# Kernel tuning notes

Hardware: AMD Instinct MI355X
Metric: run time of the kernel (lower is better)

Reference implementation:

```python
import jax, jax.numpy as jnp
import numpy as np

TOP_K = 2

def _expert(x, w1, w2, w3):
    return (jax.nn.silu(x @ w1.T) * (x @ w3.T)) @ w2.T

def setup_inputs() -> dict:
    key = jax.random.key(0)
    ks = jax.random.split(key, 8)
    B, L, D, F, E, S = 4, 2048, 1024, 512, 16, 1
    p = lambda k, shape: (jax.random.normal(k, shape, jnp.float32) * 0.02)
    return {
        "x": jax.random.normal(ks[0], (B, L, D), jnp.float32),
        "gate_w": p(ks[1], (E, D)),
        "expert_bias": jnp.zeros((E,), jnp.float32),
        "sw1": p(ks[2], (S, F, D)),
        "sw2": p(ks[3], (S, D, F)),
        "sw3": p(ks[4], (S, F, D)),
        "ew1": p(ks[5], (E, F, D)),
        "ew2": p(ks[6], (E, D, F)),
        "ew3": p(ks[7], (E, F, D)),
    }

def reference(x, gate_w, expert_bias, sw1, sw2, sw3, ew1, ew2, ew3):
    B, L, D = x.shape
    E = gate_w.shape[0]
    flat_x = x.reshape(-1, D)  # [T, D], T = B*L

    # Shared experts (always-on)
    shared = sum(_expert(flat_x, sw1[i], sw2[i], sw3[i]) for i in range(sw1.shape[0]))

    # Router (eval mode: no jitter noise, no bias update; expert_bias buffer added)
    logits = flat_x @ gate_w.T + expert_bias          # [T, E]
    probs = jax.nn.softmax(logits, axis=-1)
    topw, topi = jax.lax.top_k(probs, TOP_K)          # [T, k]
    topw = topw / jnp.sum(topw, axis=-1, keepdims=True)

    # Routed experts: combine weight per (token, expert); zero weight => zero contribution,
    # identical math to the masked gather/scatter in the original.
    out = jnp.zeros_like(flat_x)
    for e in range(E):  # fixed small structural loop over experts
        cw = jnp.sum(jnp.where(topi == e, topw, 0.0), axis=-1)  # [T]
        out = out + cw[:, None] * _expert(flat_x, ew1[e], ew2[e], ew3[e])

    y = (shared + out).reshape(B, L, D)
    return y, probs
```

## Files before the change

### kernel.cpp

```cpp
#include <hip/hip_runtime.h>

typedef unsigned short u16;
typedef __bf16 bf16_t;
typedef bf16_t bf16x8 __attribute__((ext_vector_type(8)));
typedef float f32x4 __attribute__((ext_vector_type(4)));

#define T_TOK 8192
#define DIM   1024
#define FF    512
#define NE    16
#define RBASE_SHARED (2 * T_TOK)
#define NROWS (RBASE_SHARED + T_TOK)
#define MAXTILES 256
#define NSEG 512

__device__ __forceinline__ u16 f2bf(float f) {
  union { float f; unsigned u; } v; v.f = f;
  unsigned r = v.u + 0x7FFFu + ((v.u >> 16) & 1u);
  return (u16)(r >> 16);
}
__device__ __forceinline__ float bf2f(u16 h) {
  union { unsigned u; float f; } v; v.u = ((unsigned)h) << 16; return v.f;
}
__device__ __forceinline__ int clampi(int v, int lo, int hi) {
  return v < lo ? lo : (v > hi ? hi : v);
}

#define GLL16(g, l) __builtin_amdgcn_global_load_lds( \
    (const __attribute__((address_space(1))) void*)(g), \
    (__attribute__((address_space(3))) void*)(l), 16, 0, 0)

#define X4   2097152
#define SW4  131072
#define EW4  2097152
#define TOT4 (X4 + 3 * SW4 + 3 * EW4)

__global__ __launch_bounds__(256) void cvt_all_kernel(
    const float* __restrict__ x, const float* __restrict__ sw1,
    const float* __restrict__ sw2, const float* __restrict__ sw3,
    const float* __restrict__ ew1, const float* __restrict__ ew2,
    const float* __restrict__ ew3,
    u16* __restrict__ xb, u16* __restrict__ sw1b, u16* __restrict__ sw2b,
    u16* __restrict__ sw3b, u16* __restrict__ ew1b, u16* __restrict__ ew2b,
    u16* __restrict__ ew3b) {
  int i = blockIdx.x * 256 + threadIdx.x;
  const float* s; u16* dst; int j;
  if (i < X4)                       { s = x;   dst = xb;   j = i; }
  else if (i < X4 + SW4)            { s = sw1; dst = sw1b; j = i - X4; }
  else if (i < X4 + 2 * SW4)        { s = sw2; dst = sw2b; j = i - (X4 + SW4); }
  else if (i < X4 + 3 * SW4)        { s = sw3; dst = sw3b; j = i - (X4 + 2 * SW4); }
  else if (i < X4 + 3 * SW4 + EW4)      { s = ew1; dst = ew1b; j = i - (X4 + 3 * SW4); }
  else if (i < X4 + 3 * SW4 + 2 * EW4)  { s = ew2; dst = ew2b; j = i - (X4 + 3 * SW4 + EW4); }
  else if (i < TOT4)                    { s = ew3; dst = ew3b; j = i - (X4 + 3 * SW4 + 2 * EW4); }
  else return;
  float4 v = reinterpret_cast<const float4*>(s)[j];
  ushort4 o;
  o.x = f2bf(v.x); o.y = f2bf(v.y); o.z = f2bf(v.z); o.w = f2bf(v.w);
  reinterpret_cast<ushort4*>(dst)[j] = o;
}

__global__ __launch_bounds__(256) void router_kernel(
    const float* __restrict__ x, const float* __restrict__ gw,
    const float* __restrict__ ebias, float* __restrict__ probs,
    int* __restrict__ topi, float* __restrict__ topw, int* __restrict__ cnt_seg) {
  __shared__ int hist[16];
  int tid = threadIdx.x;
  int lane = tid & 63, w = tid >> 6;
  if (tid < 16) hist[tid] = 0;
  __syncthreads();
  const float4* gv = reinterpret_cast<const float4*>(gw);
  for (int it = 0; it < 2; ++it) {
    int t0 = blockIdx.x * 16 + (w + 4 * it) * 2;
    const float4* x0 = reinterpret_cast<const float4*>(x + (size_t)t0 * DIM);
    const float4* x1 = reinterpret_cast<const float4*>(x + (size_t)(t0 + 1) * DIM);
    float4 xa[4], xc[4];
#pragma unroll
    for (int j = 0; j < 4; ++j) { xa[j] = x0[j * 64 + lane]; xc[j] = x1[j * 64 + lane]; }
    float p0[16], p1[16];
#pragma unroll
    for (int e = 0; e < NE; ++e) {
      float s0 = 0.f, s1 = 0.f;
#pragma unroll
      for (int j = 0; j < 4; ++j) {
        float4 g = gv[e * 256 + j * 64 + lane];
        s0 += xa[j].x * g.x + xa[j].y * g.y + xa[j].z * g.z + xa[j].w * g.w;
        s1 += xc[j].x * g.x + xc[j].y * g.y + xc[j].z * g.z + xc[j].w * g.w;
      }
#pragma unroll
      for (int d = 1; d < 64; d <<= 1) { s0 += __shfl_xor(s0, d); s1 += __shfl_xor(s1, d); }
      float b = ebias[e];
      p0[e] = s0 + b; p1[e] = s1 + b;
    }
    float m0 = p0[0], m1 = p1[0];
#pragma unroll
    for (int e = 1; e < NE; ++e) { m0 = fmaxf(m0, p0[e]); m1 = fmaxf(m1, p1[e]); }
    float sum0 = 0.f, sum1 = 0.f;
#pragma unroll
    for (int e = 0; e < NE; ++e) {
      p0[e] = __expf(p0[e] - m0); sum0 += p0[e];
      p1[e] = __expf(p1[e] - m1); sum1 += p1[e];
    }
    float inv0 = 1.f / sum0, inv1 = 1.f / sum1;
#pragma unroll
    for (int e = 0; e < NE; ++e) { p0[e] *= inv0; p1[e] *= inv1; }
    if (lane == 0) {
#pragma unroll
      for (int j = 0; j < 4; ++j)
        reinterpret_cast<float4*>(probs + (size_t)t0 * NE)[j] =
            make_float4(p0[4 * j], p0[4 * j + 1], p0[4 * j + 2], p0[4 * j + 3]);
      float b1 = -1.f, b2 = -1.f; int i1 = 0, i2 = 0;
#pragma unroll
      for (int e = 0; e < NE; ++e) {
        float pe = p0[e];
        if (pe > b1) { b2 = b1; i2 = i1; b1 = pe; i1 = e; }
        else if (pe > b2) { b2 = pe; i2 = e; }
      }
      float ws = b1 + b2;
      reinterpret_cast<int2*>(topi)[t0] = make_int2(i1, i2);
      reinterpret_cast<float2*>(topw)[t0] = make_float2(b1 / ws, b2 / ws);
      atomicAdd(&hist[i1], 1); atomicAdd(&hist[i2], 1);
    }
    if (lane == 1) {
      int t1 = t0 + 1;
#pragma unroll
      for (int j = 0; j < 4; ++j)
        reinterpret_cast<float4*>(probs + (size_t)t1 * NE)[j] =
            make_float4(p1[4 * j], p1[4 * j + 1], p1[4 * j + 2], p1[4 * j + 3]);
      float b1 = -1.f, b2 = -1.f; int i1 = 0, i2 = 0;
#pragma unroll
      for (int e = 0; e < NE; ++e) {
        float pe = p1[e];
        if (pe > b1) { b2 = b1; i2 = i1; b1 = pe; i1 = e; }
        else if (pe > b2) { b2 = pe; i2 = e; }
      }
      float ws = b1 + b2;
      reinterpret_cast<int2*>(topi)[t1] = make_int2(i1, i2);
      reinterpret_cast<float2*>(topw)[t1] = make_float2(b1 / ws, b2 / ws);
      atomicAdd(&hist[i1], 1); atomicAdd(&hist[i2], 1);
    }
  }
  __syncthreads();
  if (tid < 16) cnt_seg[blockIdx.x * 16 + tid] = hist[tid];
}

__global__ __launch_bounds__(256) void scan_kernel(
    const int* __restrict__ cnt_seg, int* __restrict__ cnt, int* __restrict__ offs,
    int* __restrict__ seg_base, int2* __restrict__ tab) {
  __shared__ int chunk_sum[16][16];
  __shared__ int chunk_base[16][16];
  __shared__ int tot[16], off_s[17];
  int tid = threadIdx.x;
  int e = tid & 15, c = tid >> 4;
  int s0 = 0;
  for (int s = 0; s < 32; ++s) s0 += cnt_seg[(c * 32 + s) * 16 + e];
  chunk_sum[c][e] = s0;
  __syncthreads();
  if (tid < 16) {
    int r = 0;
    for (int c2 = 0; c2 < 16; ++c2) { chunk_base[c2][tid] = r; r += chunk_sum[c2][tid]; }
    tot[tid] = r;
  }
  __syncthreads();
  if (tid == 0) {
    int a = 0;
    for (int i = 0; i < 16; ++i) { off_s[i] = a; offs[i] = a; cnt[i] = tot[i]; a += tot[i]; }
    off_s[16] = RBASE_SHARED; offs[16] = RBASE_SHARED;
    int n = 0;
    for (int g = 0; g <= 16 && n < MAXTILES; ++g) {
      int M = (g == 16) ? T_TOK : tot[g];
      for (int m0 = 0; m0 < M && n < MAXTILES; m0 += 128) { tab[n] = make_int2(g, m0); ++n; }
    }
    for (; n < MAXTILES; ++n) tab[n] = make_int2(-1, 0);
  }
  __syncthreads();
  int r = off_s[e] + chunk_base[c][e];
  for (int s = 0; s < 32; ++s) {
    int seg = c * 32 + s;
    seg_base[seg * 16 + e] = r;
    r += cnt_seg[seg * 16 + e];
  }
}

__global__ __launch_bounds__(64) void scatter_kernel(
    const int* __restrict__ topi, const float* __restrict__ topw,
    const int* __restrict__ seg_base,
    int* __restrict__ idx, float* __restrict__ cwl, int* __restrict__ slotmap) {
  __shared__ int ti[16][2]; __shared__ float tw[16][2]; __shared__ int base[16];
  int b = blockIdx.x;
  int tid = threadIdx.x;
  if (tid < 16) {
    int t = b * 16 + tid;
    int2 pp = reinterpret_cast<const int2*>(topi)[t];
    ti[tid][0] = clampi(pp.x, 0, 15); ti[tid][1] = clampi(pp.y, 0, 15);
    float2 ww = reinterpret_cast<const float2*>(topw)[t];
    tw[tid][0] = ww.x; tw[tid][1] = ww.y;
    base[tid] = seg_base[b * 16 + tid];
  }
  __syncthreads();
  if (tid < 32) {
    int l = tid >> 1, s = tid & 1;
    int t = b * 16 + l;
    int e = ti[l][s];
    int rank = 0;
    for (int t2 = 0; t2 < 16; ++t2) {
      if (ti[t2][0] == e && (t2 < l || (t2 == l && 0 < s))) ++rank;
      if (ti[t2][1] == e && (t2 < l)) ++rank;
    }
    int slot = clampi(base[e] + rank, 0, NROWS - 1);
    idx[slot] = t; cwl[slot] = tw[l][s]; slotmap[t * 3 + s] = slot;
  } else if (tid < 48) {
    int l = tid - 32;
    int t = b * 16 + l;
    int sh = RBASE_SHARED + t;
    idx[sh] = t; cwl[sh] = 1.0f; slotmap[t * 3 + 2] = sh;
  }
}

__global__ __launch_bounds__(256) void gemm_silu_kernel(
    const u16* __restrict__ A, const u16* __restrict__ sw1b, const u16* __restrict__ sw3b,
    const u16* __restrict__ ew1b, const u16* __restrict__ ew3b, u16* __restrict__ G,
    const int2* __restrict__ tab, const int* __restrict__ offs,
    const int* __restrict__ cnt, const int* __restrict__ gidx) {
  const int K = DIM;
  int nwg = gridDim.x * gridDim.y;
  int orig = blockIdx.x + gridDim.x * blockIdx.y;
  int per = nwg >> 3;
  int wg = (orig & 7) * per + (orig >> 3);
  int tileid = wg & (MAXTILES - 1);
  int ny = wg >> 8;
  int2 te = tab[tileid];
  int e = te.x;
  if (e < 0) return;
  e = clampi(e, 0, NE);
  int m0 = te.y;
  int M = (e == NE) ? T_TOK : cnt[e];
  M = clampi(M, 1, T_TOK);
  int rowbase = clampi(offs[e], 0, NROWS - 1);
  const u16* B1 = (e == NE) ? sw1b : ew1b + (size_t)e * FF * K;
  const u16* B3 = (e == NE) ? sw3b : ew3b + (size_t)e * FF * K;
  int n0 = ny * 128;

  __shared__ u16 As[2 * 4096], B1s[2 * 4096], B3s[2 * 4096];

  int tid = threadIdx.x;
  int lane = tid & 63, wv = tid >> 6;
  int srow = tid >> 2, sg = tid & 3;
  int sk0 = (sg ^ ((srow >> 1) & 3)) * 8;
  int sk1 = (sg ^ (((srow + 64) >> 1) & 3)) * 8;
  int r0 = min(m0 + srow, M - 1);
  int r1 = min(m0 + srow + 64, M - 1);
  int ga0 = clampi(gidx[clampi(rowbase + r0, 0, NROWS - 1)], 0, T_TOK - 1);
  int ga1 = clampi(gidx[clampi(rowbase + r1, 0, NROWS - 1)], 0, T_TOK - 1);
  const u16* Ap0 = A + (size_t)ga0 * K + sk0;
  const u16* Ap1 = A + (size_t)ga1 * K + sk1;
  const u16* B1p0 = B1 + (size_t)(n0 + srow) * K + sk0;
  const u16* B1p1 = B1 + (size_t)(n0 + srow + 64) * K + sk1;
  const u16* B3p0 = B3 + (size_t)(n0 + srow) * K + sk0;
  const u16* B3p1 = B3 + (size_t)(n0 + srow + 64) * K + sk1;
  int st0 = wv * 512, st1 = 2048 + wv * 512;

  int ln15 = lane & 15, qd = lane >> 4;
  int qsw = (qd ^ ((ln15 >> 1) & 3)) * 8;
  int wm = (wv >> 1) * 64, wn = (wv & 1) * 64;
  int aoff = (wm + ln15) * 32 + qsw;
  int boff = (wn + ln15) * 32 + qsw;

  f32x4 acc1[4][4] = {};
  f32x4 acc3[4][4] = {};

  const int nk = K / 32;
  GLL16(Ap0, As + st0);        GLL16(Ap1, As + st1);
  GLL16(B1p0, B1s + st0);      GLL16(B1p1, B1s + st1);
  GLL16(B3p0, B3s + st0);      GLL16(B3p1, B3s + st1);
  __syncthreads();
#pragma unroll 2
  for (int t = 0; t < nk; ++t) {
    int cur = (t & 1) * 4096;
    if (t + 1 < nk) {
      int nxt = ((t + 1) & 1) * 4096;
      int kt = (t + 1) * 32;
      GLL16(Ap0 + kt, As + nxt + st0);     GLL16(Ap1 + kt, As + nxt + st1);
      GLL16(B1p0 + kt, B1s + nxt + st0);   GLL16(B1p1 + kt, B1s + nxt + st1);
      GLL16(B3p0 + kt, B3s + nxt + st0);   GLL16(B3p1 + kt, B3s + nxt + st1);
    }
    bf16x8 af[4], b1f[4], b3f[4];
#pragma unroll
    for (int i = 0; i < 4; ++i) {
      af[i]  = *reinterpret_cast<const bf16x8*>(&As[cur + aoff + i * 512]);
      b1f[i] = *reinterpret_cast<const bf16x8*>(&B1s[cur + boff + i * 512]);
      b3f[i] = *reinterpret_cast<const bf16x8*>(&B3s[cur + boff + i * 512]);
    }
#pragma unroll
    for (int i = 0; i < 4; ++i)
#pragma unroll
      for (int j = 0; j < 4; ++j) {
        acc1[i][j] = __builtin_amdgcn_mfma_f32_16x16x32_bf16(af[i], b1f[j], acc1[i][j], 0, 0, 0);
        acc3[i][j] = __builtin_amdgcn_mfma_f32_16x16x32_bf16(af[i], b3f[j], acc3[i][j], 0, 0, 0);
      }
    __syncthreads();
  }

  int mrem = M - m0;
#pragma unroll
  for (int i = 0; i < 4; ++i)
#pragma unroll
    for (int r = 0; r < 4; ++r) {
      int ml = wm + i * 16 + qd * 4 + r;
      if (ml < mrem) {
        size_t orow = (size_t)clampi(rowbase + m0 + ml, 0, NROWS - 1);
#pragma unroll
        for (int j = 0; j < 4; ++j) {
          float z1 = acc1[i][j][r], z3 = acc3[i][j][r];
          float g = z1 / (1.f + __expf(-z1)) * z3;
          G[orow * FF + n0 + wn + j * 16 + ln15] = f2bf(g);
        }
      }
    }
}

__global__ __launch_bounds__(256) void gemm_out_kernel(
    const u16* __restrict__ Gb, const u16* __restrict__ sw2b, const u16* __restrict__ ew2b,
    u16* __restrict__ O, const int2* __restrict__ tab, const int* __restrict__ offs,
    const int* __restrict__ cnt, const float* __restrict__ cwl) {
  const int K = FF;
  int nwg = gridDim.x * gridDim.y;
  int orig = blockIdx.x + gridDim.x * blockIdx.y;
  int per = nwg >> 3;
  int wg = (orig & 7) * per + (orig >> 3);
  int tileid = wg & (MAXTILES - 1);
  int ny = wg >> 8;
  int2 te = tab[tileid];
  int e = te.x;
  if (e < 0) return;
  e = clampi(e, 0, NE);
  int m0 = te.y;
  int M = (e == NE) ? T_TOK : cnt[e];
  M = clampi(M, 1, T_TOK);
  int rowbase = clampi(offs[e], 0, NROWS - 1);
  const u16* B = (e == NE) ? sw2b : ew2b + (size_t)e * DIM * K;
  int n0 = ny * 128;

  __shared__ u16 As[2 * 4096], Bs[2 * 4096];

  int tid = threadIdx.x;
  int lane = tid & 63, wv = tid >> 6;
  int srow = tid >> 2, sg = tid & 3;
  int sk0 = (sg ^ ((srow >> 1) & 3)) * 8;
  int sk1 = (sg ^ (((srow + 64) >> 1) & 3)) * 8;
  int r0 = clampi(rowbase + min(m0 + srow, M - 1), 0, NROWS - 1);
  int r1 = clampi(rowbase + min(m0 + srow + 64, M - 1), 0, NROWS - 1);
  const u16* Ap0 = Gb + (size_t)r0 * K + sk0;
  const u16* Ap1 = Gb + (size_t)r1 * K + sk1;
  const u16* Bp0 = B + (size_t)(n0 + srow) * K + sk0;
  const u16* Bp1 = B + (size_t)(n0 + srow + 64) * K + sk1;
  int st0 = wv * 512, st1 = 2048 + wv * 512;

  int ln15 = lane & 15, qd = lane >> 4;
  int qsw = (qd ^ ((ln15 >> 1) & 3)) * 8;
  int wm = (wv >> 1) * 64, wn = (wv & 1) * 64;
  int aoff = (wm + ln15) * 32 + qsw;
  int boff = (wn + ln15) * 32 + qsw;

  f32x4 acc[4][4] = {};

  const int nk = K / 32;
  GLL16(Ap0, As + st0);    GLL16(Ap1, As + st1);
  GLL16(Bp0, Bs + st0);    GLL16(Bp1, Bs + st1);
  __syncthreads();
#pragma unroll 2
  for (int t = 0; t < nk; ++t) {
    int cur = (t & 1) * 4096;
    if (t + 1 < nk) {
      int nxt = ((t + 1) & 1) * 4096;
      int kt = (t + 1) * 32;
      GLL16(Ap0 + kt, As + nxt + st0);   GLL16(Ap1 + kt, As + nxt + st1);
      GLL16(Bp0 + kt, Bs + nxt + st0);   GLL16(Bp1 + kt, Bs + nxt + st1);
    }
    bf16x8 af[4], bf[4];
#pragma unroll
    for (int i = 0; i < 4; ++i) {
      af[i] = *reinterpret_cast<const bf16x8*>(&As[cur + aoff + i * 512]);
      bf[i] = *reinterpret_cast<const bf16x8*>(&Bs[cur + boff + i * 512]);
    }
#pragma unroll
    for (int i = 0; i < 4; ++i)
#pragma unroll
      for (int j = 0; j < 4; ++j)
        acc[i][j] = __builtin_amdgcn_mfma_f32_16x16x32_bf16(af[i], bf[j], acc[i][j], 0, 0, 0);
    __syncthreads();
  }

  int mrem = M - m0;
#pragma unroll
  for (int i = 0; i < 4; ++i)
#pragma unroll
    for (int r = 0; r < 4; ++r) {
      int ml = wm + i * 16 + qd * 4 + r;
      if (ml < mrem) {
        int slot = clampi(rowbase + m0 + ml, 0, NROWS - 1);
        float cw = cwl[slot];
#pragma unroll
        for (int j = 0; j < 4; ++j)
          O[(size_t)slot * DIM + n0 + wn + j * 16 + ln15] = f2bf(acc[i][j][r] * cw);
      }
    }
}

__global__ __launch_bounds__(256) void combine_kernel(
    const u16* __restrict__ O, const int* __restrict__ slotmap, float* __restrict__ y) {
  int t = blockIdx.x;
  int c = threadIdx.x;
  int s0 = clampi(slotmap[t * 3], 0, NROWS - 1);
  int s1 = clampi(slotmap[t * 3 + 1], 0, NROWS - 1);
  int s2 = clampi(slotmap[t * 3 + 2], 0, NROWS - 1);
  ushort4 a = reinterpret_cast<const ushort4*>(O + (size_t)s0 * DIM)[c];
  ushort4 b = reinterpret_cast<const ushort4*>(O + (size_t)s1 * DIM)[c];
  ushort4 d = reinterpret_cast<const ushort4*>(O + (size_t)s2 * DIM)[c];
  float4 r;
  r.x = bf2f(a.x) + bf2f(b.x) + bf2f(d.x);
  r.y = bf2f(a.y) + bf2f(b.y) + bf2f(d.y);
  r.z = bf2f(a.z) + bf2f(b.z) + bf2f(d.z);
  r.w = bf2f(a.w) + bf2f(b.w) + bf2f(d.w);
  reinterpret_cast<float4*>(y + (size_t)t * DIM)[c] = r;
}

extern "C" void kernel_launch(void* const* d_in, const int* in_sizes, int n_in,
                              void* d_out, int out_size, void* d_ws, size_t ws_size,
                              hipStream_t stream) {
  const float* x     = (const float*)d_in[0];
  const float* gw    = (const float*)d_in[1];
  const float* ebias = (const float*)d_in[2];
  const float* sw1   = (const float*)d_in[3];
  const float* sw2   = (const float*)d_in[4];
  const float* sw3   = (const float*)d_in[5];
  const float* ew1   = (const float*)d_in[6];
  const float* ew2   = (const float*)d_in[7];
  const float* ew3   = (const float*)d_in[8];
  float* y = (float*)d_out;
  float* probs = y + (size_t)T_TOK * DIM;

  char* ws = (char*)d_ws;
  size_t o = 0;
  auto alloc = [&](size_t bytes) -> char* {
    char* p = ws + o;
    o = (o + bytes + 255) & ~(size_t)255;
    return p;
  };
  u16* G    = (u16*)alloc((size_t)NROWS * FF * 2);
  u16* sw1b = (u16*)alloc((size_t)FF * DIM * 2);
  u16* sw2b = (u16*)alloc((size_t)FF * DIM * 2);
  u16* sw3b = (u16*)alloc((size_t)FF * DIM * 2);
  u16* ew2b = (u16*)alloc((size_t)NE * FF * DIM * 2);
  char* aliasBase = alloc((size_t)NROWS * DIM * 2);
  u16* xb   = (u16*)aliasBase;
  u16* ew1b = (u16*)(aliasBase + (size_t)T_TOK * DIM * 2);
  u16* ew3b = (u16*)(aliasBase + (size_t)T_TOK * DIM * 2 + (size_t)NE * FF * DIM * 2);
  u16* O    = (u16*)aliasBase;
  int*   topi    = (int*)alloc(T_TOK * 2 * 4);
  float* topw    = (float*)alloc(T_TOK * 2 * 4);
  int*   idx     = (int*)alloc(NROWS * 4);
  float* cwl     = (float*)alloc(NROWS * 4);
  int*   slotmap = (int*)alloc(T_TOK * 3 * 4);
  int2*  tab     = (int2*)alloc(MAXTILES * 8);
  int*   cnt_seg = (int*)alloc(NSEG * 16 * 4);
  int*   seg_base= (int*)alloc(NSEG * 16 * 4);
  int*   cnt     = (int*)alloc(256);
  int*   offs    = (int*)alloc(256);

  router_kernel<<<NSEG, 256, 0, stream>>>(x, gw, ebias, probs, topi, topw, cnt_seg);
  scan_kernel<<<1, 256, 0, stream>>>(cnt_seg, cnt, offs, seg_base, tab);
  scatter_kernel<<<NSEG, 64, 0, stream>>>(topi, topw, seg_base, idx, cwl, slotmap);
  cvt_all_kernel<<<TOT4 / 256, 256, 0, stream>>>(x, sw1, sw2, sw3, ew1, ew2, ew3,
                                                 xb, sw1b, sw2b, sw3b, ew1b, ew2b, ew3b);

  gemm_silu_kernel<<<dim3(MAXTILES, 4, 1), 256, 0, stream>>>(
      xb, sw1b, sw3b, ew1b, ew3b, G, tab, offs, cnt, idx);
  gemm_out_kernel<<<dim3(MAXTILES, 8, 1), 256, 0, stream>>>(
      G, sw2b, ew2b, O, tab, offs, cnt, cwl);
  combine_kernel<<<T_TOK, 256, 0, stream>>>(O, slotmap, y);
}
```

Before: 449.0 us.

## Restructure GEMM mainloops with two-stage async prefetch and explicit vmcnt barriers

Both grouped GEMM kernels now prefetch two K-tiles up front. Each iteration waits on vmcnt for only the older tile, reads fragments into registers, then issues the next global-to-LDS load into the freed buffer before running the MFMAs. This replaces the single __syncthreads per step with finer s_waitcnt/s_barrier control so loads overlap compute more fully. The workgroup-to-tile remapping is also changed to interleave tiles across XCDs differently. The inline-asm waits depend on the compiler not reordering LDS traffic, which sched_barrier is meant to enforce.

```diff
diff --git a/kernel.cpp b/kernel.cpp
--- a/kernel.cpp
+++ b/kernel.cpp
@@ -29,6 +29,10 @@
 #define GLL16(g, l) __builtin_amdgcn_global_load_lds( \
     (const __attribute__((address_space(1))) void*)(g), \
     (__attribute__((address_space(3))) void*)(l), 16, 0, 0)
+
+#define WAIT_VM_BARRIER(n) asm volatile("s_waitcnt vmcnt(" #n ")\n\ts_barrier" ::: "memory")
+#define BARRIER_ONLY()     asm volatile("s_barrier" ::: "memory")
+#define WAIT_LGKM0()       asm volatile("s_waitcnt lgkmcnt(0)" ::: "memory")
 
 #define X4   2097152
 #define SW4  131072
@@ -222,12 +226,10 @@
     const int2* __restrict__ tab, const int* __restrict__ offs,
     const int* __restrict__ cnt, const int* __restrict__ gidx) {
   const int K = DIM;
-  int nwg = gridDim.x * gridDim.y;
   int orig = blockIdx.x + gridDim.x * blockIdx.y;
-  int per = nwg >> 3;
-  int wg = (orig & 7) * per + (orig >> 3);
-  int tileid = wg & (MAXTILES - 1);
-  int ny = wg >> 8;
+  int xcd = orig & 7, q = orig >> 3;
+  int tileid = xcd + 8 * (q & 31);
+  int ny = q >> 5;
   int2 te = tab[tileid];
   int e = te.x;
   if (e < 0) return;
@@ -269,20 +271,16 @@
   f32x4 acc3[4][4] = {};
 
   const int nk = K / 32;
-  GLL16(Ap0, As + st0);        GLL16(Ap1, As + st1);
-  GLL16(B1p0, B1s + st0);      GLL16(B1p1, B1s + st1);
-  GLL16(B3p0, B3s + st0);      GLL16(B3p1, B3s + st1);
-  __syncthreads();
-#pragma unroll 2
-  for (int t = 0; t < nk; ++t) {
+  GLL16(Ap0, As + st0);            GLL16(Ap1, As + st1);
+  GLL16(B1p0, B1s + st0);          GLL16(B1p1, B1s + st1);
+  GLL16(B3p0, B3s + st0);          GLL16(B3p1, B3s + st1);
+  GLL16(Ap0 + 32, As + 4096 + st0);    GLL16(Ap1 + 32, As + 4096 + st1);
+  GLL16(B1p0 + 32, B1s + 4096 + st0);  GLL16(B1p1 + 32, B1s + 4096 + st1);
+  GLL16(B3p0 + 32, B3s + 4096 + st0);  GLL16(B3p1 + 32, B3s + 4096 + st1);
+
+  for (int t = 0; t < nk - 2; ++t) {
     int cur = (t & 1) * 4096;
-    if (t + 1 < nk) {
-      int nxt = ((t + 1) & 1) * 4096;
-      int kt = (t + 1) * 32;
-      GLL16(Ap0 + kt, As + nxt + st0);     GLL16(Ap1 + kt, As + nxt + st1);
-      GLL16(B1p0 + kt, B1s + nxt + st0);   GLL16(B1p1 + kt, B1s + nxt + st1);
-      GLL16(B3p0 + kt, B3s + nxt + st0);   GLL16(B3p1 + kt, B3s + nxt + st1);
-    }
+    WAIT_VM_BARRIER(6);
     bf16x8 af[4], b1f[4], b3f[4];
 #pragma unroll
     for (int i = 0; i < 4; ++i) {
@@ -290,6 +288,13 @@
       b1f[i] = *reinterpret_cast<const bf16x8*>(&B1s[cur + boff + i * 512]);
       b3f[i] = *reinterpret_cast<const bf16x8*>(&B3s[cur + boff + i * 512]);
     }
+    WAIT_LGKM0();
+    __builtin_amdgcn_sched_barrier(0);
+    BARRIER_ONLY();
+    int kt = (t + 2) * 32;
+    GLL16(Ap0 + kt, As + cur + st0);     GLL16(Ap1 + kt, As + cur + st1);
+    GLL16(B1p0 + kt, B1s + cur + st0);   GLL16(B1p1 + kt, B1s + cur + st1);
+    GLL16(B3p0 + kt, B3s + cur + st0);   GLL16(B3p1 + kt, B3s + cur + st1);
 #pragma unroll
     for (int i = 0; i < 4; ++i)
 #pragma unroll
@@ -297,7 +302,46 @@
         acc1[i][j] = __builtin_amdgcn_mfma_f32_16x16x32_bf16(af[i], b1f[j], acc1[i][j], 0, 0, 0);
         acc3[i][j] = __builtin_amdgcn_mfma_f32_16x16x32_bf16(af[i], b3f[j], acc3[i][j], 0, 0, 0);
       }
-    __syncthreads();
+  }
+  {
+    int cur = ((nk - 2) & 1) * 4096;
+    WAIT_VM_BARRIER(6);
+    bf16x8 af[4], b1f[4], b3f[4];
+#pragma unroll
+    for (int i = 0; i < 4; ++i) {
+      af[i]  = *reinterpret_cast<const bf16x8*>(&As[cur + aoff + i * 512]);
+      b1f[i] = *reinterpret_cast<const bf16x8*>(&B1s[cur + boff + i * 512]);
+      b3f[i] = *reinterpret_cast<const bf16x8*>(&B3s[cur + boff + i * 512]);
+    }
+    WAIT_LGKM0();
+    __builtin_amdgcn_sched_barrier(0);
+#pragma unroll
+    for (int i = 0; i < 4; ++i)
+#pragma unroll
+      for (int j = 0; j < 4; ++j) {
+        acc1[i][j] = __builtin_amdgcn_mfma_f32_16x16x32_bf16(af[i], b1f[j], acc1[i][j], 0, 0, 0);
+        acc3[i][j] = __builtin_amdgcn_mfma_f32_16x16x32_bf16(af[i], b3f[j], acc3[i][j], 0, 0, 0);
+      }
+  }
+  {
+    int cur = ((nk - 1) & 1) * 4096;
+    WAIT_VM_BARRIER(0);
+    bf16x8 af[4], b1f[4], b3f[4];
+#pragma unroll
+    for (int i = 0; i < 4; ++i) {
+      af[i]  = *reinterpret_cast<const bf16x8*>(&As[cur + aoff + i * 512]);
+      b1f[i] = *reinterpret_cast<const bf16x8*>(&B1s[cur + boff + i * 512]);
+      b3f[i] = *reinterpret_cast<const bf16x8*>(&B3s[cur + boff + i * 512]);
+    }
+    WAIT_LGKM0();
+    __builtin_amdgcn_sched_barrier(0);
+#pragma unroll
+    for (int i = 0; i < 4; ++i)
+#pragma unroll
+      for (int j = 0; j < 4; ++j) {
+        acc1[i][j] = __builtin_amdgcn_mfma_f32_16x16x32_bf16(af[i], b1f[j], acc1[i][j], 0, 0, 0);
+        acc3[i][j] = __builtin_amdgcn_mfma_f32_16x16x32_bf16(af[i], b3f[j], acc3[i][j], 0, 0, 0);
+      }
   }
 
   int mrem = M - m0;
@@ -323,12 +367,10 @@
     u16* __restrict__ O, const int2* __restrict__ tab, const int* __restrict__ offs,
     const int* __restrict__ cnt, const float* __restrict__ cwl) {
   const int K = FF;
-  int nwg = gridDim.x * gridDim.y;
   int orig = blockIdx.x + gridDim.x * blockIdx.y;
-  int per = nwg >> 3;
-  int wg = (orig & 7) * per + (orig >> 3);
-  int tileid = wg & (MAXTILES - 1);
-  int ny = wg >> 8;
+  int xcd = orig & 7, q = orig >> 3;
+  int tileid = xcd + 8 * (q & 31);
+  int ny = q >> 5;
   int2 te = tab[tileid];
   int e = te.x;
   if (e < 0) return;
@@ -366,28 +408,63 @@
   const int nk = K / 32;
   GLL16(Ap0, As + st0);    GLL16(Ap1, As + st1);
   GLL16(Bp0, Bs + st0);    GLL16(Bp1, Bs + st1);
-  __syncthreads();
-#pragma unroll 2
-  for (int t = 0; t < nk; ++t) {
+  GLL16(Ap0 + 32, As + 4096 + st0);  GLL16(Ap1 + 32, As + 4096 + st1);
+  GLL16(Bp0 + 32, Bs + 4096 + st0);  GLL16(Bp1 + 32, Bs + 4096 + st1);
+
+  for (int t = 0; t < nk - 2; ++t) {
     int cur = (t & 1) * 4096;
-    if (t + 1 < nk) {
-      int nxt = ((t + 1) & 1) * 4096;
-      int kt = (t + 1) * 32;
-      GLL16(Ap0 + kt, As + nxt + st0);   GLL16(Ap1 + kt, As + nxt + st1);
-      GLL16(Bp0 + kt, Bs + nxt + st0);   GLL16(Bp1 + kt, Bs + nxt + st1);
-    }
+    WAIT_VM_BARRIER(4);
     bf16x8 af[4], bf[4];
 #pragma unroll
     for (int i = 0; i < 4; ++i) {
       af[i] = *reinterpret_cast<const bf16x8*>(&As[cur + aoff + i * 512]);
       bf[i] = *reinterpret_cast<const bf16x8*>(&Bs[cur + boff + i * 512]);
     }
+    WAIT_LGKM0();
+    __builtin_amdgcn_sched_barrier(0);
+    BARRIER_ONLY();
+    int kt = (t + 2) * 32;
+    GLL16(Ap0 + kt, As + cur + st0);   GLL16(Ap1 + kt, As + cur + st1);
+    GLL16(Bp0 + kt, Bs + cur + st0);   GLL16(Bp1 + kt, Bs + cur + st1);
 #pragma unroll
     for (int i = 0; i < 4; ++i)
 #pragma unroll
       for (int j = 0; j < 4; ++j)
         acc[i][j] = __builtin_amdgcn_mfma_f32_16x16x32_bf16(af[i], bf[j], acc[i][j], 0, 0, 0);
-    __syncthreads();
+  }
+  {
+    int cur = ((nk - 2) & 1) * 4096;
+    WAIT_VM_BARRIER(4);
+    bf16x8 af[4], bf[4];
+#pragma unroll
+    for (int i = 0; i < 4; ++i) {
+      af[i] = *reinterpret_cast<const bf16x8*>(&As[cur + aoff + i * 512]);
+      bf[i] = *reinterpret_cast<const bf16x8*>(&Bs[cur + boff + i * 512]);
+    }
+    WAIT_LGKM0();
+    __builtin_amdgcn_sched_barrier(0);
+#pragma unroll
+    for (int i = 0; i < 4; ++i)
+#pragma unroll
+      for (int j = 0; j < 4; ++j)
+        acc[i][j] = __builtin_amdgcn_mfma_f32_16x16x32_bf16(af[i], bf[j], acc[i][j], 0, 0, 0);
+  }
+  {
+    int cur = ((nk - 1) & 1) * 4096;
+    WAIT_VM_BARRIER(0);
+    bf16x8 af[4], bf[4];
+#pragma unroll
+    for (int i = 0; i < 4; ++i) {
+      af[i] = *reinterpret_cast<const bf16x8*>(&As[cur + aoff + i * 512]);
+      bf[i] = *reinterpret_cast<const bf16x8*>(&Bs[cur + boff + i * 512]);
+    }
+    WAIT_LGKM0();
+    __builtin_amdgcn_sched_barrier(0);
+#pragma unroll
+    for (int i = 0; i < 4; ++i)
+#pragma unroll
+      for (int j = 0; j < 4; ++j)
+        acc[i][j] = __builtin_amdgcn_mfma_f32_16x16x32_bf16(af[i], bf[j], acc[i][j], 0, 0, 0);
   }
 
   int mrem = M - m0;
```

Result: no change. 443.7 us (-1.2%).
